# Optimization experiments

Measured on AMD Instinct MI355X. Metric: run time of the kernel, lower is better.

The kernel has to match this reference:

```python
import jax, jax.numpy as jnp
import numpy as np

NEG = -1000000000.0  # matches torch masked_fill value

def setup_inputs() -> dict:
    key = jax.random.key(0)
    ks = jax.random.split(key, 9)
    B, S, T, Din, Dout = 8, 16, 128, 64, 64
    x = jax.random.normal(ks[0], (B, S, T, Din), dtype=jnp.float32)
    # tags_mask[b,s] = 1 if tag in {'C1','ASSBS_C1','NC1'} else 0
    tags_mask = jax.random.randint(ks[1], (B, S), 0, 2).astype(jnp.int32)
    mask = jnp.ones((T, T), dtype=jnp.float32)  # base time-time mask
    sc = 1.0 / np.sqrt(Din)
    Wk_w = jax.random.normal(ks[2], (Dout, Din), dtype=jnp.float32) * sc
    Wk_b = jax.random.normal(ks[3], (Dout,), dtype=jnp.float32) * 0.01
    Wq_w = jax.random.normal(ks[4], (Dout, Din), dtype=jnp.float32) * sc
    Wq_b = jax.random.normal(ks[5], (Dout,), dtype=jnp.float32) * 0.01
    Wv_w = jax.random.normal(ks[6], (Dout, Din), dtype=jnp.float32) * sc
    Wv_b = jax.random.normal(ks[7], (Dout,), dtype=jnp.float32) * 0.01
    return {"x": x, "tags_mask": tags_mask, "mask": mask,
            "Wk_w": Wk_w, "Wk_b": Wk_b, "Wq_w": Wq_w, "Wq_b": Wq_b,
            "Wv_w": Wv_w, "Wv_b": Wv_b}

def reference(x, tags_mask, mask, Wk_w, Wk_b, Wq_w, Wq_b, Wv_w, Wv_b):
    B, S, T, _ = x.shape
    d = Wq_w.shape[0]
    # QKV projections (torch Linear: x @ W.T + b)
    k = x @ Wk_w.T + Wk_b  # [B,S,T,d]
    q = x @ Wq_w.T + Wq_b
    v = x @ Wv_w.T + Wv_b
    qf = q.reshape(B, S * T, d)
    kf = k.reshape(B, S * T, d)
    scores = jnp.einsum('bnd,bmd->bnm', qf, kf) / jnp.sqrt(jnp.asarray(d, scores_dtype := q.dtype))
    # tag mask: (b,s,t) attends to (b,s',t') iff base[t,t'] and same C1-group(s,s')
    same = tags_mask[:, :, None] == tags_mask[:, None, :]          # [B,S,S]
    base = mask != 0                                               # [T,T]
    full = (same[:, :, None, :, None] & base[None, None, :, None, :]).reshape(B, S * T, S * T)
    scores = jnp.where(full, scores, NEG)
    p_attn = jax.nn.softmax(scores, axis=-1)                       # [B,ST,ST]
    # dropout(p=0.5) is identity in eval mode
    # faithful quirk: value is transposed to [B,T,S,d] before flattening
    vf = v.transpose(0, 2, 1, 3).reshape(B, T * S, d)
    ctx = jnp.einsum('bnm,bmd->bnd', p_attn, vf).reshape(B, S, T, d)
    return ctx, p_attn
```

## Files before the change

### kernel.cpp

```cpp
#include <hip/hip_runtime.h>
#include <stdint.h>

#define B_   8
#define S_   16
#define T_   128
#define D_   64
#define N_   2048
#define NEGV (-1000000000.0f)

typedef short s16x8 __attribute__((ext_vector_type(8)));
typedef float f32x4 __attribute__((ext_vector_type(4)));

static __device__ __forceinline__ unsigned short f2bf(float f) {
    unsigned u = __builtin_bit_cast(unsigned, f);
    u += 0x7FFFu + ((u >> 16) & 1u);
    return (unsigned short)(u >> 16);
}
static __device__ __forceinline__ float bf2f(unsigned short h) {
    unsigned u = ((unsigned)h) << 16;
    return __builtin_bit_cast(float, u);
}
static __device__ __forceinline__ s16x8 ldfrag_g(const unsigned short* p) {
    uint4 v = *(const uint4*)p;
    return __builtin_bit_cast(s16x8, v);
}
static __device__ __forceinline__ s16x8 ldfrag_l(const unsigned short* p) {
    uint4 v = *(const uint4*)p;
    return __builtin_bit_cast(s16x8, v);
}

__global__ __launch_bounds__(256, 2) void proj_kernel(
    const float* __restrict__ x,
    const float* __restrict__ Wq, const float* __restrict__ bq,
    const float* __restrict__ Wk, const float* __restrict__ bk,
    const float* __restrict__ Wv, const float* __restrict__ bv,
    unsigned short* __restrict__ qb, unsigned short* __restrict__ kb,
    unsigned short* __restrict__ vbT)
{
    __shared__ unsigned short xs[64][72];
    __shared__ unsigned short Wl[192][72];
    __shared__ float          biasl[192];

    const int tid = threadIdx.x;
    const int g0  = blockIdx.x * 64;

    const float4* xsrc = (const float4*)(x + (size_t)g0 * 64);
    #pragma unroll
    for (int k2 = 0; k2 < 4; ++k2) {
        int idx = tid + 256 * k2;
        float4 v = xsrc[idx];
        int tok = idx >> 4, i4 = (idx & 15) * 4;
        uint2 pk;
        pk.x = (unsigned)f2bf(v.x) | ((unsigned)f2bf(v.y) << 16);
        pk.y = (unsigned)f2bf(v.z) | ((unsigned)f2bf(v.w) << 16);
        *(uint2*)&xs[tok][i4] = pk;
    }
    #pragma unroll
    for (int k2 = 0; k2 < 12; ++k2) {
        const float* wsrc = (k2 < 4) ? Wq : ((k2 < 8) ? Wk : Wv);
        int f4i = (k2 & 3) * 256 + tid;
        float4 v = ((const float4*)wsrc)[f4i];
        int j = f4i >> 4, i4 = (f4i & 15) * 4;
        int row = (k2 >> 2) * 64 + j;
        uint2 pk;
        pk.x = (unsigned)f2bf(v.x) | ((unsigned)f2bf(v.y) << 16);
        pk.y = (unsigned)f2bf(v.z) | ((unsigned)f2bf(v.w) << 16);
        *(uint2*)&Wl[row][i4] = pk;
    }
    if (tid < 192) {
        int m = tid >> 6;
        const float* bs = (m == 0) ? bq : (m == 1 ? bk : bv);
        biasl[tid] = bs[tid & 63];
    }
    __syncthreads();

    const int w = tid >> 6, lane = tid & 63;
    const int q = lane >> 4, l15 = lane & 15;

    #pragma unroll
    for (int e = 0; e < 3; ++e) {
        const int nt   = w * 3 + e;
        const int matU = nt >> 2;
        const float bsc = biasl[nt * 16 + l15];
        const float scl = (matU == 0) ? 0.125f : 1.0f;
        const int j = (nt & 3) * 16 + l15;
        unsigned short* dqk = (matU == 0) ? qb : kb;
        #pragma unroll
        for (int ms = 0; ms < 4; ++ms) {
            f32x4 acc = {0.f, 0.f, 0.f, 0.f};
            #pragma unroll
            for (int ks = 0; ks < 2; ++ks) {
                s16x8 a = ldfrag_l(&xs[ms * 16 + l15][ks * 32 + q * 8]);
                s16x8 b = ldfrag_l(&Wl[nt * 16 + l15][ks * 32 + q * 8]);
                acc = __builtin_amdgcn_mfma_f32_16x16x32_bf16(a, b, acc, 0, 0, 0);
            }
            #pragma unroll
            for (int r = 0; r < 4; ++r) {
                int tok = ms * 16 + 4 * q + r;
                int g = g0 + tok;
                unsigned short h = f2bf((acc[r] + bsc) * scl);
                if (matU < 2) {
                    dqk[(size_t)g * 64 + j] = h;
                } else {
                    int b = g >> 11, n = g & (N_ - 1);
                    int s = n >> 7,  t = n & (T_ - 1);
                    vbT[((size_t)b * 64 + j) * N_ + t * S_ + s] = h;
                }
            }
        }
    }
}

__global__ __launch_bounds__(256, 2) void attn_kernel(
    const unsigned short* __restrict__ qb,
    const unsigned short* __restrict__ kb,
    const unsigned short* __restrict__ vbT,
    const int*  __restrict__ tags,
    const float* __restrict__ mask,
    float* __restrict__ out)
{
    __shared__ unsigned short plds[4][16][136];
    __shared__ float ctxbuf[4][16][64];
    __shared__ unsigned maskcols[128];
    __shared__ float lsum[4][16];
    __shared__ float ltinv[16];

    const int tid = threadIdx.x;
    const int bb  = blockIdx.x >> 7;
    const int q0  = (blockIdx.x & 127) * 16;
    const int s   = q0 >> 7;
    const int t0  = q0 & (T_ - 1);

    if (tid < 128) {
        unsigned bits = 0;
        #pragma unroll
        for (int i = 0; i < 16; ++i)
            bits |= (mask[(t0 + i) * T_ + tid] != 0.0f ? 1u : 0u) << i;
        maskcols[tid] = bits;
    }
    __syncthreads();

    const int w = tid >> 6, lane = tid & 63;
    const int q = lane >> 4, l15 = lane & 15;
    const int col0w = w * 512;

    unsigned mbq[8];
    #pragma unroll
    for (int nt = 0; nt < 8; ++nt)
        mbq[nt] = (maskcols[nt * 16 + l15] >> (4 * q)) & 0xFu;

    const int tg = tags[bb * S_ + s];

    const unsigned short* qrow = qb + ((size_t)bb * N_ + q0 + l15) * 64 + q * 8;
    const s16x8 aq0 = ldfrag_g(qrow);
    const s16x8 aq1 = ldfrag_g(qrow + 32);

    float ps[4] = {0.f, 0.f, 0.f, 0.f};
    f32x4 pvacc[4];
    #pragma unroll
    for (int nv = 0; nv < 4; ++nv) pvacc[nv] = (f32x4){0.f, 0.f, 0.f, 0.f};

    unsigned stash[4][16];
    bool validt[4];
    float* pbase = out + (size_t)(B_ * N_ * 64);

    #pragma unroll
    for (int tile = 0; tile < 4; ++tile) {
        const int colT = col0w + tile * 128;
        const bool valid = (tags[bb * S_ + (colT >> 7)] == tg);
        validt[tile] = valid;
        if (valid) {
            f32x4 sacc[8];
            #pragma unroll
            for (int nt = 0; nt < 8; ++nt) sacc[nt] = (f32x4){0.f, 0.f, 0.f, 0.f};
            const unsigned short* kB =
                kb + ((size_t)bb * N_ + colT + l15) * 64 + q * 8;
            #pragma unroll
            for (int nt = 0; nt < 8; ++nt) {
                s16x8 b0 = ldfrag_g(kB + nt * (16 * 64));
                s16x8 b1 = ldfrag_g(kB + nt * (16 * 64) + 32);
                sacc[nt] = __builtin_amdgcn_mfma_f32_16x16x32_bf16(aq0, b0, sacc[nt], 0, 0, 0);
                sacc[nt] = __builtin_amdgcn_mfma_f32_16x16x32_bf16(aq1, b1, sacc[nt], 0, 0, 0);
            }
            #pragma unroll
            for (int nt = 0; nt < 8; ++nt) {
                float e[4];
                #pragma unroll
                for (int r = 0; r < 4; ++r) {
                    float sc = ((mbq[nt] >> r) & 1u) ? sacc[nt][r] : NEGV;
                    e[r] = __expf(sc);
                    ps[r] += e[r];
                    plds[w][4 * q + r][nt * 16 + l15] = f2bf(e[r]);
                }
                stash[tile][nt * 2 + 0] = (unsigned)f2bf(e[0]) | ((unsigned)f2bf(e[1]) << 16);
                stash[tile][nt * 2 + 1] = (unsigned)f2bf(e[2]) | ((unsigned)f2bf(e[3]) << 16);
            }
        } else {
            #pragma unroll
            for (int jj = 0; jj < 8; ++jj) {
                int idx = jj * 64 + lane;
                int row = idx >> 5, c4 = (idx & 31) * 4;
                float4 z = {0.f, 0.f, 0.f, 0.f};
                *(float4*)(pbase + ((size_t)bb * N_ + q0 + row) * N_ + colT + c4) = z;
            }
        }
        __syncthreads();
        if (valid) {
            #pragma unroll
            for (int ks = 0; ks < 4; ++ks) {
                s16x8 ap = ldfrag_l(&plds[w][l15][ks * 32 + q * 8]);
                #pragma unroll
                for (int nv = 0; nv < 4; ++nv) {
                    const unsigned short* vB =
                        vbT + ((size_t)bb * 64 + nv * 16 + l15) * N_ + colT + ks * 32 + q * 8;
                    s16x8 bv = ldfrag_g(vB);
                    pvacc[nv] = __builtin_amdgcn_mfma_f32_16x16x32_bf16(ap, bv, pvacc[nv], 0, 0, 0);
                }
            }
        }
    }

    #pragma unroll
    for (int r = 0; r < 4; ++r) {
        float v = ps[r];
        v += __shfl_xor(v, 1);
        v += __shfl_xor(v, 2);
        v += __shfl_xor(v, 4);
        v += __shfl_xor(v, 8);
        ps[r] = v;
    }
    if (l15 == 0) {
        float4 pv = {ps[0], ps[1], ps[2], ps[3]};
        *(float4*)&lsum[w][4 * q] = pv;
    }
    #pragma unroll
    for (int nv = 0; nv < 4; ++nv)
        #pragma unroll
        for (int r = 0; r < 4; ++r)
            ctxbuf[w][4 * q + r][nv * 16 + l15] = pvacc[nv][r];
    __syncthreads();

    float inv[4];
    #pragma unroll
    for (int r = 0; r < 4; ++r) {
        float lt = lsum[0][4 * q + r] + lsum[1][4 * q + r] +
                   lsum[2][4 * q + r] + lsum[3][4 * q + r];
        inv[r] = 1.0f / lt;
    }
    if (w == 0 && l15 == 0) {
        #pragma unroll
        for (int r = 0; r < 4; ++r) ltinv[4 * q + r] = inv[r];
    }

    #pragma unroll
    for (int tile = 0; tile < 4; ++tile) {
        if (!validt[tile]) continue;
        const int colT = col0w + tile * 128;
        float* prow = pbase + ((size_t)bb * N_ + q0 + 4 * q) * N_ + colT + l15;
        #pragma unroll
        for (int nt = 0; nt < 8; ++nt) {
            unsigned p01 = stash[tile][nt * 2 + 0];
            unsigned p23 = stash[tile][nt * 2 + 1];
            prow[0 * N_ + nt * 16] = bf2f((unsigned short)(p01 & 0xFFFFu)) * inv[0];
            prow[1 * N_ + nt * 16] = bf2f((unsigned short)(p01 >> 16))     * inv[1];
            prow[2 * N_ + nt * 16] = bf2f((unsigned short)(p23 & 0xFFFFu)) * inv[2];
            prow[3 * N_ + nt * 16] = bf2f((unsigned short)(p23 >> 16))     * inv[3];
        }
    }
    __syncthreads();

    #pragma unroll
    for (int e = 0; e < 4; ++e) {
        int idx = tid + 256 * e;
        int row = idx >> 6, dv = idx & 63;
        float v = ctxbuf[0][row][dv] + ctxbuf[1][row][dv] +
                  ctxbuf[2][row][dv] + ctxbuf[3][row][dv];
        v *= ltinv[row];
        out[((size_t)bb * N_ + q0 + row) * 64 + dv] = v;
    }
}

extern "C" void kernel_launch(void* const* d_in, const int* in_sizes, int n_in,
                              void* d_out, int out_size, void* d_ws, size_t ws_size,
                              hipStream_t stream)
{
    (void)in_sizes; (void)n_in; (void)out_size; (void)ws_size;
    const float* x    = (const float*)d_in[0];
    const int*   tags = (const int*)  d_in[1];
    const float* mask = (const float*)d_in[2];
    const float* Wk   = (const float*)d_in[3];
    const float* bk   = (const float*)d_in[4];
    const float* Wq   = (const float*)d_in[5];
    const float* bq   = (const float*)d_in[6];
    const float* Wv   = (const float*)d_in[7];
    const float* bv   = (const float*)d_in[8];
    float* out = (float*)d_out;

    unsigned short* qbuf = (unsigned short*)d_ws;
    unsigned short* kbuf = qbuf + (size_t)B_ * N_ * 64;
    unsigned short* vbT  = kbuf + (size_t)B_ * N_ * 64;

    hipLaunchKernelGGL(proj_kernel, dim3(256), dim3(256), 0, stream,
                       x, Wq, bq, Wk, bk, Wv, bv, qbuf, kbuf, vbT);
    hipLaunchKernelGGL(attn_kernel, dim3(B_ * (N_ / 16)), dim3(256), 0, stream,
                       qbuf, kbuf, vbT, tags, mask, out);
}
```

Before: 198.7 us.

## Coalesce p_attn stores through LDS transpose and drop per-tile block barriers

Removes the block-wide __syncthreads inside the tile loop, since each wave only reads its own plds slice, and moves the zero-fill of invalid tiles to the end of the kernel. The normalized probability write now stages the bf16 stash back into LDS and emits row-contiguous float4 stores in place of scattered scalar stores. The LDS row pitch is padded from 136 to 138 halfwords. This targets the 128 MB p_attn write, which dominates runtime. The cost is extra LDS traffic, and it depends on correct intra-wave ordering of LDS accesses now that the per-tile barrier is gone.

Result: faster. 192.8 us (-3.0%).

```diff
diff --git a/kernel.cpp b/kernel.cpp
--- a/kernel.cpp
+++ b/kernel.cpp
@@ -119,7 +119,7 @@
     const float* __restrict__ mask,
     float* __restrict__ out)
 {
-    __shared__ unsigned short plds[4][16][136];
+    __shared__ unsigned short plds[4][16][138];
     __shared__ float ctxbuf[4][16][64];
     __shared__ unsigned maskcols[128];
     __shared__ float lsum[4][16];
@@ -169,53 +169,44 @@
         const int colT = col0w + tile * 128;
         const bool valid = (tags[bb * S_ + (colT >> 7)] == tg);
         validt[tile] = valid;
-        if (valid) {
-            f32x4 sacc[8];
-            #pragma unroll
-            for (int nt = 0; nt < 8; ++nt) sacc[nt] = (f32x4){0.f, 0.f, 0.f, 0.f};
-            const unsigned short* kB =
-                kb + ((size_t)bb * N_ + colT + l15) * 64 + q * 8;
-            #pragma unroll
-            for (int nt = 0; nt < 8; ++nt) {
-                s16x8 b0 = ldfrag_g(kB + nt * (16 * 64));
-                s16x8 b1 = ldfrag_g(kB + nt * (16 * 64) + 32);
-                sacc[nt] = __builtin_amdgcn_mfma_f32_16x16x32_bf16(aq0, b0, sacc[nt], 0, 0, 0);
-                sacc[nt] = __builtin_amdgcn_mfma_f32_16x16x32_bf16(aq1, b1, sacc[nt], 0, 0, 0);
-            }
-            #pragma unroll
-            for (int nt = 0; nt < 8; ++nt) {
-                float e[4];
-                #pragma unroll
-                for (int r = 0; r < 4; ++r) {
-                    float sc = ((mbq[nt] >> r) & 1u) ? sacc[nt][r] : NEGV;
-                    e[r] = __expf(sc);
-                    ps[r] += e[r];
-                    plds[w][4 * q + r][nt * 16 + l15] = f2bf(e[r]);
-                }
-                stash[tile][nt * 2 + 0] = (unsigned)f2bf(e[0]) | ((unsigned)f2bf(e[1]) << 16);
-                stash[tile][nt * 2 + 1] = (unsigned)f2bf(e[2]) | ((unsigned)f2bf(e[3]) << 16);
-            }
-        } else {
-            #pragma unroll
-            for (int jj = 0; jj < 8; ++jj) {
-                int idx = jj * 64 + lane;
-                int row = idx >> 5, c4 = (idx & 31) * 4;
-                float4 z = {0.f, 0.f, 0.f, 0.f};
-                *(float4*)(pbase + ((size_t)bb * N_ + q0 + row) * N_ + colT + c4) = z;
-            }
-        }
-        __syncthreads();
-        if (valid) {
-            #pragma unroll
-            for (int ks = 0; ks < 4; ++ks) {
-                s16x8 ap = ldfrag_l(&plds[w][l15][ks * 32 + q * 8]);
-                #pragma unroll
-                for (int nv = 0; nv < 4; ++nv) {
-                    const unsigned short* vB =
-                        vbT + ((size_t)bb * 64 + nv * 16 + l15) * N_ + colT + ks * 32 + q * 8;
-                    s16x8 bv = ldfrag_g(vB);
-                    pvacc[nv] = __builtin_amdgcn_mfma_f32_16x16x32_bf16(ap, bv, pvacc[nv], 0, 0, 0);
-                }
+        if (!valid) continue;
+
+        f32x4 sacc[8];
+        #pragma unroll
+        for (int nt = 0; nt < 8; ++nt) sacc[nt] = (f32x4){0.f, 0.f, 0.f, 0.f};
+        const unsigned short* kB =
+            kb + ((size_t)bb * N_ + colT + l15) * 64 + q * 8;
+        #pragma unroll
+        for (int nt = 0; nt < 8; ++nt) {
+            s16x8 b0 = ldfrag_g(kB + nt * (16 * 64));
+            s16x8 b1 = ldfrag_g(kB + nt * (16 * 64) + 32);
+            sacc[nt] = __builtin_amdgcn_mfma_f32_16x16x32_bf16(aq0, b0, sacc[nt], 0, 0, 0);
+            sacc[nt] = __builtin_amdgcn_mfma_f32_16x16x32_bf16(aq1, b1, sacc[nt], 0, 0, 0);
+        }
+        #pragma unroll
+        for (int nt = 0; nt < 8; ++nt) {
+            float e[4];
+            unsigned short h[4];
+            #pragma unroll
+            for (int r = 0; r < 4; ++r) {
+                float sc = ((mbq[nt] >> r) & 1u) ? sacc[nt][r] : NEGV;
+                e[r] = __expf(sc);
+                ps[r] += e[r];
+                h[r] = f2bf(e[r]);
+                plds[w][4 * q + r][nt * 16 + l15] = h[r];
+            }
+            stash[tile][nt * 2 + 0] = (unsigned)h[0] | ((unsigned)h[1] << 16);
+            stash[tile][nt * 2 + 1] = (unsigned)h[2] | ((unsigned)h[3] << 16);
+        }
+        #pragma unroll
+        for (int ks = 0; ks < 4; ++ks) {
+            s16x8 ap = ldfrag_l(&plds[w][l15][ks * 32 + q * 8]);
+            #pragma unroll
+            for (int nv = 0; nv < 4; ++nv) {
+                const unsigned short* vB =
+                    vbT + ((size_t)bb * 64 + nv * 16 + l15) * N_ + colT + ks * 32 + q * 8;
+                s16x8 bv = ldfrag_g(vB);
+                pvacc[nv] = __builtin_amdgcn_mfma_f32_16x16x32_bf16(ap, bv, pvacc[nv], 0, 0, 0);
             }
         }
     }
@@ -240,34 +231,49 @@
             ctxbuf[w][4 * q + r][nv * 16 + l15] = pvacc[nv][r];
     __syncthreads();
 
-    float inv[4];
-    #pragma unroll
-    for (int r = 0; r < 4; ++r) {
-        float lt = lsum[0][4 * q + r] + lsum[1][4 * q + r] +
-                   lsum[2][4 * q + r] + lsum[3][4 * q + r];
-        inv[r] = 1.0f / lt;
-    }
-    if (w == 0 && l15 == 0) {
-        #pragma unroll
-        for (int r = 0; r < 4; ++r) ltinv[4 * q + r] = inv[r];
-    }
+    if (tid < 16) {
+        float lt = lsum[0][tid] + lsum[1][tid] + lsum[2][tid] + lsum[3][tid];
+        ltinv[tid] = 1.0f / lt;
+    }
+    __syncthreads();
 
     #pragma unroll
     for (int tile = 0; tile < 4; ++tile) {
-        if (!validt[tile]) continue;
         const int colT = col0w + tile * 128;
-        float* prow = pbase + ((size_t)bb * N_ + q0 + 4 * q) * N_ + colT + l15;
-        #pragma unroll
-        for (int nt = 0; nt < 8; ++nt) {
-            unsigned p01 = stash[tile][nt * 2 + 0];
-            unsigned p23 = stash[tile][nt * 2 + 1];
-            prow[0 * N_ + nt * 16] = bf2f((unsigned short)(p01 & 0xFFFFu)) * inv[0];
-            prow[1 * N_ + nt * 16] = bf2f((unsigned short)(p01 >> 16))     * inv[1];
-            prow[2 * N_ + nt * 16] = bf2f((unsigned short)(p23 & 0xFFFFu)) * inv[2];
-            prow[3 * N_ + nt * 16] = bf2f((unsigned short)(p23 >> 16))     * inv[3];
-        }
-    }
-    __syncthreads();
+        if (validt[tile]) {
+            #pragma unroll
+            for (int nt = 0; nt < 8; ++nt) {
+                unsigned p01 = stash[tile][nt * 2 + 0];
+                unsigned p23 = stash[tile][nt * 2 + 1];
+                plds[w][4 * q + 0][nt * 16 + l15] = (unsigned short)(p01 & 0xFFFFu);
+                plds[w][4 * q + 1][nt * 16 + l15] = (unsigned short)(p01 >> 16);
+                plds[w][4 * q + 2][nt * 16 + l15] = (unsigned short)(p23 & 0xFFFFu);
+                plds[w][4 * q + 3][nt * 16 + l15] = (unsigned short)(p23 >> 16);
+            }
+            #pragma unroll
+            for (int j = 0; j < 8; ++j) {
+                int idx = j * 64 + lane;
+                int row = idx >> 5;
+                int c4  = (idx & 31) * 4;
+                uint2 hv = *(const uint2*)&plds[w][row][c4];
+                float iv = ltinv[row];
+                float4 o;
+                o.x = bf2f((unsigned short)(hv.x & 0xFFFFu)) * iv;
+                o.y = bf2f((unsigned short)(hv.x >> 16))     * iv;
+                o.z = bf2f((unsigned short)(hv.y & 0xFFFFu)) * iv;
+                o.w = bf2f((unsigned short)(hv.y >> 16))     * iv;
+                *(float4*)(pbase + ((size_t)bb * N_ + q0 + row) * N_ + colT + c4) = o;
+            }
+        } else {
+            #pragma unroll
+            for (int j = 0; j < 8; ++j) {
+                int idx = j * 64 + lane;
+                int row = idx >> 5, c4 = (idx & 31) * 4;
+                float4 z = {0.f, 0.f, 0.f, 0.f};
+                *(float4*)(pbase + ((size_t)bb * N_ + q0 + row) * N_ + colT + c4) = z;
+            }
+        }
+    }
 
     #pragma unroll
     for (int e = 0; e < 4; ++e) {
```
